# Optimization experiments

Measured on AMD Instinct MI355X. Metric: run time of the kernel, lower is better.

## Reference

```python
import jax, jax.numpy as jnp
import numpy as np

N = 131072          # total nodes per batched graph side
E = 524288          # total edges per batched graph side (avg degree 4)
B = 4096            # number of graph pairs
NPG = 32            # nodes per graph
NEG_SLOPE = 0.2
LN_EPS = 1e-5


def setup_inputs() -> dict:
    key = jax.random.key(0)
    ks = jax.random.split(key, 40)
    rn = lambda k, s, sc=0.05: jax.random.normal(k, s, dtype=jnp.float32) * sc
    inp = {}
    inp["feat1"] = jax.random.normal(ks[0], (N, 6), dtype=jnp.float32)
    inp["feat2"] = jax.random.normal(ks[1], (N, 6), dtype=jnp.float32)
    inp["llm_emb"] = jax.random.normal(ks[2], (B, 1024), dtype=jnp.float32)
    inp["src1"] = jax.random.randint(ks[3], (E,), 0, N, dtype=jnp.int32)
    inp["dst1"] = jax.random.randint(ks[4], (E,), 0, N, dtype=jnp.int32)
    inp["src2"] = jax.random.randint(ks[5], (E,), 0, N, dtype=jnp.int32)
    inp["dst2"] = jax.random.randint(ks[6], (E,), 0, N, dtype=jnp.int32)
    inp["gid"] = (jnp.arange(N, dtype=jnp.int32) // NPG).astype(jnp.int32)
    # shared GAT weights (layer: W[in,H*Dh], attn_l[H,Dh], attn_r[H,Dh], bias[H*Dh])
    inp["W1"] = rn(ks[7], (6, 128));   inp["al1"] = rn(ks[8], (4, 32));  inp["ar1"] = rn(ks[9], (4, 32));  inp["b1"] = rn(ks[10], (128,))
    inp["W2"] = rn(ks[11], (128, 128)); inp["al2"] = rn(ks[12], (4, 32)); inp["ar2"] = rn(ks[13], (4, 32)); inp["b2"] = rn(ks[14], (128,))
    inp["W3"] = rn(ks[15], (128, 256)); inp["al3"] = rn(ks[16], (4, 64)); inp["ar3"] = rn(ks[17], (4, 64)); inp["b3"] = rn(ks[18], (256,))
    # fusion
    inp["Wpg"] = rn(ks[19], (512, 512)); inp["bpg"] = rn(ks[20], (512,))
    inp["Wpl"] = rn(ks[21], (1024, 512)); inp["bpl"] = rn(ks[22], (512,))
    inp["Wv"] = rn(ks[23], (512, 512));  inp["bv"] = rn(ks[24], (512,))
    inp["Wo"] = rn(ks[25], (512, 512));  inp["bo"] = rn(ks[26], (512,))
    inp["gamma"] = jnp.ones((512,), jnp.float32); inp["beta"] = jnp.zeros((512,), jnp.float32)
    # classifier
    inp["Wc1"] = rn(ks[27], (512, 256)); inp["bc1"] = rn(ks[28], (256,))
    inp["Wc2"] = rn(ks[29], (256, 1));   inp["bc2"] = rn(ks[30], (1,))
    return inp


def _gat(x, src, dst, W, al, ar, b):
    # DGL GATConv: e_ij = LeakyReLU(a_l.h_src + a_r.h_dst), softmax over edges per dst
    H, Dh = al.shape
    h = (x @ W).reshape(-1, H, Dh)                 # [N,H,Dh]
    el = jnp.sum(h * al, axis=-1)                  # [N,H]
    er = jnp.sum(h * ar, axis=-1)                  # [N,H]
    e = jax.nn.leaky_relu(el[src] + er[dst], NEG_SLOPE)   # [E,H]
    m = jax.ops.segment_max(e, dst, num_segments=N)
    a = jnp.exp(e - m[dst])
    s = jax.ops.segment_sum(a, dst, num_segments=N)
    alpha = a / jnp.where(s[dst] == 0, 1.0, s[dst])       # [E,H]
    out = jax.ops.segment_sum(alpha[:, :, None] * h[src], dst, num_segments=N)
    return out.reshape(-1, H * Dh) + b


def _gnn(x, src, dst, gid, W1, al1, ar1, b1, W2, al2, ar2, b2, W3, al3, ar3, b3):
    h = jax.nn.relu(_gat(x, src, dst, W1, al1, ar1, b1))
    h = jax.nn.relu(_gat(h, src, dst, W2, al2, ar2, b2))
    h = _gat(h, src, dst, W3, al3, ar3, b3)        # [N,256]
    sums = jax.ops.segment_sum(h, gid, num_segments=B)
    cnt = jax.ops.segment_sum(jnp.ones((h.shape[0], 1), h.dtype), gid, num_segments=B)
    return sums / cnt                               # [B,256] mean_nodes


def reference(feat1, feat2, llm_emb, src1, dst1, src2, dst2, gid,
              W1, al1, ar1, b1, W2, al2, ar2, b2, W3, al3, ar3, b3,
              Wpg, bpg, Wpl, bpl, Wv, bv, Wo, bo, gamma, beta,
              Wc1, bc1, Wc2, bc2):
    h1 = _gnn(feat1, src1, dst1, gid, W1, al1, ar1, b1, W2, al2, ar2, b2, W3, al3, ar3, b3)
    h2 = _gnn(feat2, src2, dst2, gid, W1, al1, ar1, b1, W2, al2, ar2, b2, W3, al3, ar3, b3)
    pair = jnp.concatenate([h1, h2], axis=1)        # [B,512]
    gp = pair @ Wpg + bpg                           # [B,512]
    lp = llm_emb @ Wpl + bpl                        # [B,512]
    # MHA with kv seq_len 1: softmax over a single key == 1 -> out = W_o(W_v gp)
    attn = (gp @ Wv + bv) @ Wo + bo
    x = attn + lp
    mu = jnp.mean(x, axis=-1, keepdims=True)
    var = jnp.mean((x - mu) ** 2, axis=-1, keepdims=True)
    fused = (x - mu) / jnp.sqrt(var + LN_EPS) * gamma + beta
    hcls = jax.nn.relu(fused @ Wc1 + bc1)
    return jax.nn.sigmoid(hcls @ Wc2 + bc2)         # [B,1]
```

## Files before the change

kernel.cpp:

```cpp
#include <hip/hip_runtime.h>
#include <hip/hip_fp8.h>

#define NN 131072
#define NE 524288
#define NB 4096
#define CAP 16
#define NEG_SLOPE 0.2f
#define LN_EPS 1e-5f
#define LOG2E 1.44269504088896f

#define NBKT 1024
#define NBLK1 256
#define CELL_CAP 24

typedef unsigned short bf16;
typedef __attribute__((ext_vector_type(8))) short short8;
typedef __attribute__((ext_vector_type(4))) float floatx4;
typedef __attribute__((ext_vector_type(2))) float floatx2;

#if __has_builtin(__builtin_amdgcn_exp2f)
#define EXP2(x) __builtin_amdgcn_exp2f(x)
#else
#define EXP2(x) exp2f(x)
#endif

__device__ __forceinline__ float bf2f(bf16 h) {
    return __uint_as_float((unsigned)h << 16);
}
__device__ __forceinline__ bf16 f2bf(float f) {
    unsigned u = __float_as_uint(f);
    unsigned r = (u + 0x7FFFu + ((u >> 16) & 1u)) >> 16;
    return (bf16)r;
}
__device__ __forceinline__ unsigned pkbf(float lo, float hi) {
    unsigned r;
    asm("v_cvt_pk_bf16_f32 %0, %1, %2" : "=v"(r) : "v"(lo), "v"(hi));
    return r;
}
__device__ __forceinline__ unsigned char ftofp8(float f) {
    return (unsigned char)(__builtin_amdgcn_cvt_pk_fp8_f32(f, f, 0, false) & 0xFF);
}
__device__ __forceinline__ float leaky(float x) {
    return fmaxf(x, 0.f) + NEG_SLOPE * fminf(x, 0.f);
}

__global__ __launch_bounds__(256) void part_edges_kernel(
        const int* __restrict__ s0, const int* __restrict__ d0,
        const int* __restrict__ s1, const int* __restrict__ d1,
        unsigned* __restrict__ cells, int* __restrict__ counts) {
    __shared__ int lcnt[NBKT];
    int blk = blockIdx.x, t = threadIdx.x;
    for (int i = t; i < NBKT; i += 256) lcnt[i] = 0;
    __syncthreads();
    int side = blk >= (NBLK1 / 2);
    const int4* dp = (const int4*)(side ? d1 : d0);
    const int4* sp = (const int4*)(side ? s1 : s0);
    int base4 = (blk - side * (NBLK1 / 2)) * 1024;
    int gbase = side * NN;
#pragma unroll
    for (int it = 0; it < 4; it++) {
        int e4 = base4 + it * 256 + t;
        int4 dd = dp[e4];
        int4 ss = sp[e4];
        int d[4] = {gbase + dd.x, gbase + dd.y, gbase + dd.z, gbase + dd.w};
        int s[4] = {gbase + ss.x, gbase + ss.y, gbase + ss.z, gbase + ss.w};
#pragma unroll
        for (int k = 0; k < 4; k++) {
            int b = d[k] >> 8;
            int r = atomicAdd(&lcnt[b], 1);
            if (r < CELL_CAP)
                cells[((size_t)b * NBLK1 + blk) * CELL_CAP + r] =
                    ((unsigned)s[k] << 8) | (unsigned)(d[k] & 255);
        }
    }
    __syncthreads();
    for (int i = t; i < NBKT; i += 256) {
        int c = lcnt[i];
        counts[i * NBLK1 + blk] = (c > CELL_CAP) ? CELL_CAP : c;
    }
}

__global__ __launch_bounds__(256) void build_slots_kernel(
        const unsigned* __restrict__ cells, const int* __restrict__ counts,
        int* __restrict__ deg, int* __restrict__ slots) {
    __shared__ int ldeg[256];
    __shared__ int lslot[256 * CAP];
    int b = blockIdx.x, t = threadIdx.x;
    ldeg[t] = 0;
    for (int i = t; i < 256 * CAP; i += 256) lslot[i] = 0;
    __syncthreads();
    int cnt = counts[b * NBLK1 + t];
    const unsigned* cp = cells + ((size_t)b * NBLK1 + t) * CELL_CAP;
    for (int i = 0; i < cnt; i++) {
        unsigned v = cp[i];
        int d = v & 255;
        int s = (int)(v >> 8);
        int p = atomicAdd(&ldeg[d], 1);
        if (p < CAP) lslot[d * CAP + p] = s;
    }
    __syncthreads();
    int node0 = b * 256;
    deg[node0 + t] = ldeg[t];
    for (int i = t; i < 256 * CAP; i += 256)
        slots[(size_t)node0 * CAP + i] = lslot[i];
}

#define PREP_TOTAL (16384 + 32768 + 524288 + 131072 + 2048 + 2048 + 48 + 4096)

__global__ void prep_all_kernel(const float* __restrict__ W2, const float* __restrict__ W3,
                                const float* __restrict__ Wpl, const float* __restrict__ Wc1,
                                const float* __restrict__ W1,
                                const float* __restrict__ al1, const float* __restrict__ ar1,
                                const float* __restrict__ al2, const float* __restrict__ ar2,
                                const float* __restrict__ al3, const float* __restrict__ ar3,
                                const float* __restrict__ b1v,
                                bf16* __restrict__ W2t, bf16* __restrict__ W3t,
                                bf16* __restrict__ Wplt, bf16* __restrict__ Wc1t,
                                bf16* __restrict__ Ff2, bf16* __restrict__ Ff3,
                                float* __restrict__ F1, bf16* __restrict__ W1f) {
    int i = blockIdx.x * blockDim.x + threadIdx.x;
    if (i < 16384) {
        int c = i >> 7, k = i & 127;
        W2t[i] = f2bf(W2[k * 128 + c]);
        return;
    }
    i -= 16384;
    if (i < 32768) {
        int c = i >> 7, k = i & 127;
        W3t[i] = f2bf(W3[k * 256 + c]);
        return;
    }
    i -= 32768;
    if (i < 524288) {
        int c = i >> 10, k = i & 1023;
        Wplt[i] = f2bf(Wpl[k * 512 + c]);
        return;
    }
    i -= 524288;
    if (i < 131072) {
        int c = i >> 9, k = i & 511;
        Wc1t[i] = f2bf(Wc1[k * 256 + c]);
        return;
    }
    i -= 131072;
    if (i < 2048) {
        int c = i >> 7, k = i & 127;
        float s = 0.f;
        if (c < 8) {
            const float* a = (c < 4) ? al2 : ar2;
            int hh = c & 3;
            for (int d = 0; d < 32; d++) s += W2[k * 128 + hh * 32 + d] * a[hh * 32 + d];
        }
        Ff2[i] = f2bf(s);
        return;
    }
    i -= 2048;
    if (i < 2048) {
        int c = i >> 7, k = i & 127;
        float s = 0.f;
        if (c < 8) {
            const float* a = (c < 4) ? al3 : ar3;
            int hh = c & 3;
            for (int d = 0; d < 64; d++) s += W3[k * 256 + hh * 64 + d] * a[hh * 64 + d];
        }
        Ff3[i] = f2bf(s);
        return;
    }
    i -= 2048;
    if (i < 48) {
        int k = i >> 3, c = i & 7;
        const float* a = (c < 4) ? al1 : ar1;
        int hh = c & 3;
        float s = 0.f;
        for (int d = 0; d < 32; d++) s += W1[k * 128 + hh * 32 + d] * a[hh * 32 + d];
        F1[k * 8 + c] = s * LOG2E;
        return;
    }
    i -= 48;
    if (i < 4096) {
        int c = i >> 5, k = i & 31;
        int h = c >> 5, d = k & 7;
        float v = 0.f;
        if ((k >> 3) == h) {
            if (d < 6) v = W1[d * 128 + c];
            else if (d == 6) v = b1v[c];
        }
        W1f[i] = f2bf(v);
    }
}

__global__ void f2bf_kernel(const float* __restrict__ x, bf16* __restrict__ y) {
    int i = blockIdx.x * blockDim.x + threadIdx.x;
    float4 v = ((const float4*)x)[i];
    ushort4 u;
    u.x = f2bf(v.x); u.y = f2bf(v.y); u.z = f2bf(v.z); u.w = f2bf(v.w);
    ((ushort4*)y)[i] = u;
}

__global__ void wt_kernel(const float* __restrict__ W, bf16* __restrict__ Wt, int K, int C) {
    int i = blockIdx.x * blockDim.x + threadIdx.x;
    if (i >= K * C) return;
    int c = i / K, k = i - c * K;
    Wt[i] = f2bf(W[(size_t)k * C + c]);
}


__global__ void featelr_kernel(const float* __restrict__ f0, const float* __restrict__ f1,
                               const float* __restrict__ F1, float* __restrict__ fpk,
                               float* __restrict__ el, float* __restrict__ er) {
    int n = blockIdx.x * blockDim.x + threadIdx.x;
    const float* x = (n < NN) ? (f0 + (size_t)n * 6) : (f1 + (size_t)(n - NN) * 6);
    float xv[6];
#pragma unroll
    for (int k = 0; k < 6; k++) xv[k] = x[k];
    float4* o = (float4*)(fpk + (size_t)n * 8);
    o[0] = make_float4(xv[0], xv[1], xv[2], xv[3]);
    o[1] = make_float4(xv[4], xv[5], 0.f, 0.f);
    float4 elv, erv;
    float* ep = (float*)&elv;
    float* rp = (float*)&erv;
#pragma unroll
    for (int c = 0; c < 4; c++) {
        float sl = 0.f, sr = 0.f;
#pragma unroll
        for (int k = 0; k < 6; k++) {
            sl += xv[k] * F1[k * 8 + c];
            sr += xv[k] * F1[k * 8 + c + 4];
        }
        ep[c] = sl;
        rp[c] = sr;
    }
    *(float4*)(el + (size_t)n * 4) = elv;
    *(float4*)(er + (size_t)n * 4) = erv;
}

__global__ __launch_bounds__(256) void agg1mfma_kernel(
        const float* __restrict__ fpk, const float* __restrict__ el,
        const float* __restrict__ er, const int* __restrict__ deg,
        const int* __restrict__ slots, const bf16* __restrict__ W1fg,
        bf16* __restrict__ xb) {
    __shared__ bf16 sW[128 * 40];
    __shared__ bf16 sagg[256 * 40];
    int t = threadIdx.x;
    if (t < 128) {
        const uint4* src = (const uint4*)(W1fg + t * 32);
        uint4* dstp = (uint4*)(sW + t * 40);
        dstp[0] = src[0]; dstp[1] = src[1]; dstp[2] = src[2]; dstp[3] = src[3];
    }

    int node = blockIdx.x * 256 + t;
    int dg = deg[node];
    dg = (dg > CAP) ? CAP : dg;
    float4 er4 = *(const float4*)(er + (size_t)node * 4);
    const int* sp = slots + (size_t)node * CAP;
    float a0[4], a1[4], a2[4], a3[4], a4[4], a5[4], ss[4];
#pragma unroll
    for (int h = 0; h < 4; h++) {
        a0[h] = a1[h] = a2[h] = a3[h] = a4[h] = a5[h] = ss[h] = 0.f;
    }
    for (int p = 0; p < dg; p += 4) {
        int4 s4 = *(const int4*)(sp + p);
        int sarr[4] = {s4.x, s4.y, s4.z, s4.w};
#pragma unroll
        for (int k = 0; k < 4; k++) {
            bool vld = (p + k) < dg;
            int g = vld ? sarr[k] : s4.x;
            float4 e4 = *(const float4*)(el + (size_t)g * 4);
            float4 xa = *(const float4*)(fpk + (size_t)g * 8);
            float4 xc = *(const float4*)(fpk + (size_t)g * 8 + 4);
            float eh[4] = {e4.x, e4.y, e4.z, e4.w};
            float rh[4] = {er4.x, er4.y, er4.z, er4.w};
#pragma unroll
            for (int h = 0; h < 4; h++) {
                float z = eh[h] + rh[h];
                float w = EXP2(fmaxf(z, 0.f) + NEG_SLOPE * fminf(z, 0.f));
                w = vld ? w : 0.f;
                ss[h] += w;
                a0[h] += w * xa.x; a1[h] += w * xa.y; a2[h] += w * xa.z;
                a3[h] += w * xa.w; a4[h] += w * xc.x; a5[h] += w * xc.y;
            }
        }
    }
#pragma unroll
    for (int h = 0; h < 4; h++) {
        float rs = (dg > 0) ? 1.f / ss[h] : 0.f;
        uint4 o;
        o.x = pkbf(a0[h] * rs, a1[h] * rs);
        o.y = pkbf(a2[h] * rs, a3[h] * rs);
        o.z = pkbf(a4[h] * rs, a5[h] * rs);
        o.w = 0x00003F80u;
        *(uint4*)(sagg + t * 40 + h * 8) = o;
    }
    __syncthreads();

    int wave = t >> 6, lane = t & 63;
    int mlane = lane & 15, quad = lane >> 4;
    short8 af[8];
#pragma unroll
    for (int j = 0; j < 8; j++)
        af[j] = *(const short8*)(sW + (j * 16 + mlane) * 40 + quad * 8);
    floatx4 z4 = (floatx4){0.f, 0.f, 0.f, 0.f};
#pragma unroll
    for (int nt = 0; nt < 4; nt++) {
        int lrow = wave * 64 + nt * 16 + mlane;
        short8 bfr = *(const short8*)(sagg + lrow * 40 + quad * 8);
        floatx4 c[8];
#pragma unroll
        for (int j = 0; j < 8; j++)
            c[j] = __builtin_amdgcn_mfma_f32_16x16x32_bf16(af[j], bfr, z4, 0, 0, 0);
        bf16* op = xb + (size_t)(blockIdx.x * 256 + lrow) * 128 + quad * 4;
#pragma unroll
        for (int j = 0; j < 8; j++) {
            uint2 o;
            o.x = pkbf(fmaxf(c[j][0], 0.f), fmaxf(c[j][1], 0.f));
            o.y = pkbf(fmaxf(c[j][2], 0.f), fmaxf(c[j][3], 0.f));
            *(uint2*)(op + j * 16) = o;
        }
    }
}


__device__ __forceinline__ void softmax_phaseA(const float* __restrict__ el,
                                               const float* __restrict__ er,
                                               const int* __restrict__ slots,
                                               int wid, int dg, int lane,
                                               float* alpha_out, int* src_out) {
    int e = lane & 15, h = lane >> 4;
    int sA = slots[(size_t)wid * CAP + e];
    int sAc = (e < dg) ? sA : 0;
    float erh = er[wid * 4 + h];
    float elv = el[sAc * 4 + h];
    float w = (e < dg) ? __expf(leaky(elv + erh)) : 0.f;
    float ssum = w;
    ssum += __shfl_xor(ssum, 1, 64);
    ssum += __shfl_xor(ssum, 2, 64);
    ssum += __shfl_xor(ssum, 4, 64);
    ssum += __shfl_xor(ssum, 8, 64);
    *alpha_out = (dg > 0) ? w * (1.f / ssum) : 0.f;
    *src_out = sAc;
}

__global__ void agg2_kernel(const unsigned char* __restrict__ h8, const float* __restrict__ el,
                            const float* __restrict__ er, const int* __restrict__ deg,
                            const int* __restrict__ slots, const float* __restrict__ bias,
                            bf16* __restrict__ out) {
    int t = blockIdx.x * blockDim.x + threadIdx.x;
    int wid = t >> 5;
    int gl = threadIdx.x & 31;
    int dg = deg[wid];
    dg = (dg > CAP) ? CAP : dg;
    int head = gl >> 3;
    int fbase = gl * 4;
    float erh = er[wid * 4 + head];
    const int* sp = slots + (size_t)wid * CAP;
    float a0 = 0.f, a1 = 0.f, a2 = 0.f, a3 = 0.f, ssum = 0.f;

    for (int p = 0; p < dg; p += 4) {
        int4 s4 = *(const int4*)(sp + p);
        int s[4]; bool v[4];
        s[0] = s4.x; v[0] = true;
        v[1] = p + 1 < dg; s[1] = v[1] ? s4.y : s4.x;
        v[2] = p + 2 < dg; s[2] = v[2] ? s4.z : s4.x;
        v[3] = p + 3 < dg; s[3] = v[3] ? s4.w : s4.x;
        float elv[4]; unsigned u1[4];
#pragma unroll
        for (int k = 0; k < 4; k++) {
            elv[k] = el[s[k] * 4 + head];
            u1[k] = *(const unsigned*)(h8 + (size_t)s[k] * 128 + fbase);
        }
#pragma unroll
        for (int k = 0; k < 4; k++) {
            float w = v[k] ? __expf(leaky(elv[k] + erh)) : 0.f;
            ssum += w;
            floatx2 lo = __builtin_amdgcn_cvt_pk_f32_fp8((int)u1[k], false);
            floatx2 hi = __builtin_amdgcn_cvt_pk_f32_fp8((int)u1[k], true);
            a0 += w * lo[0]; a1 += w * lo[1];
            a2 += w * hi[0]; a3 += w * hi[1];
        }
    }
    float rs = (dg > 0) ? 1.f / ssum : 0.f;
    float4 bbv = *(const float4*)(bias + fbase);
    float v0 = fmaxf(a0 * rs + bbv.x, 0.f), v1 = fmaxf(a1 * rs + bbv.y, 0.f);
    float v2 = fmaxf(a2 * rs + bbv.z, 0.f), v3 = fmaxf(a3 * rs + bbv.w, 0.f);
    uint2 uo;
    uo.x = (unsigned)f2bf(v0) | ((unsigned)f2bf(v1) << 16);
    uo.y = (unsigned)f2bf(v2) | ((unsigned)f2bf(v3) << 16);
    *(uint2*)(out + (size_t)wid * 128 + fbase) = uo;
}

__global__ void agg3pool_kernel(const unsigned char* __restrict__ h8,
                                const float* __restrict__ el, const float* __restrict__ er,
                                const int* __restrict__ deg, const int* __restrict__ slots,
                                const float* __restrict__ bias, bf16* __restrict__ pair) {
    __shared__ float red[4 * 256];
    int side = blockIdx.x >> 12;
    int b = blockIdx.x & 4095;
    int nodebase = side * NN + b * 32;
    int grp = threadIdx.x >> 6, lane = threadIdx.x & 63;
    int fbase = lane * 4;
    int grpbase = lane & 48;
    float p0 = 0.f, p1 = 0.f, p2 = 0.f, p3 = 0.f;

    for (int nn = 0; nn < 8; nn++) {
        int wid = nodebase + grp * 8 + nn;
        int dg = deg[wid];
        dg = (dg > CAP) ? CAP : dg;
        float alpha; int sAc;
        softmax_phaseA(el, er, slots, wid, dg, lane, &alpha, &sAc);
        for (int p = 0; p < dg; p += 4) {
            int sc[4]; float av[4];
#pragma unroll
            for (int k = 0; k < 4; k++) {
                int srcl = grpbase + p + k;
                sc[k] = __shfl(sAc, srcl, 64);
                av[k] = __shfl(alpha, srcl, 64);
            }
            unsigned u[4];
#pragma unroll
            for (int k = 0; k < 4; k++)
                u[k] = *(const unsigned*)(h8 + (size_t)sc[k] * 256 + fbase);
#pragma unroll
            for (int k = 0; k < 4; k++) {
                floatx2 lo = __builtin_amdgcn_cvt_pk_f32_fp8((int)u[k], false);
                floatx2 hi = __builtin_amdgcn_cvt_pk_f32_fp8((int)u[k], true);
                p0 += av[k] * lo[0]; p1 += av[k] * lo[1];
                p2 += av[k] * hi[0]; p3 += av[k] * hi[1];
            }
        }
    }
    red[grp * 256 + fbase + 0] = p0;
    red[grp * 256 + fbase + 1] = p1;
    red[grp * 256 + fbase + 2] = p2;
    red[grp * 256 + fbase + 3] = p3;
    __syncthreads();
    if (grp == 0) {
        float4 bbv = *(const float4*)(bias + fbase);
        float s0 = 0.f, s1 = 0.f, s2 = 0.f, s3 = 0.f;
#pragma unroll
        for (int g = 0; g < 4; g++) {
            s0 += red[g * 256 + fbase + 0];
            s1 += red[g * 256 + fbase + 1];
            s2 += red[g * 256 + fbase + 2];
            s3 += red[g * 256 + fbase + 3];
        }
        const float inv = 1.0f / 32.0f;
        float v0 = s0 * inv + bbv.x, v1 = s1 * inv + bbv.y;
        float v2 = s2 * inv + bbv.z, v3 = s3 * inv + bbv.w;
        uint2 uo;
        uo.x = (unsigned)f2bf(v0) | ((unsigned)f2bf(v1) << 16);
        uo.y = (unsigned)f2bf(v2) | ((unsigned)f2bf(v3) << 16);
        *(uint2*)(pair + (size_t)b * 512 + side * 256 + fbase) = uo;
    }
}

template <bool FOLD, bool OUT8>
__global__ __launch_bounds__(256) void mgemm_kernel(const bf16* __restrict__ A,
                                                    const bf16* __restrict__ Wt,
                                                    const float* __restrict__ bias,
                                                    void* __restrict__ out,
                                                    int K, int C, int relu,
                                                    const bf16* __restrict__ Ff,
                                                    float* __restrict__ el,
                                                    float* __restrict__ er) {
    __shared__ short As[128 * 48];
    __shared__ short Bs[128 * 48];
    int t = threadIdx.x;
    int wave = t >> 6, lane = t & 63;
    int wm = (wave >> 1) * 64, wn = (wave & 1) * 64;
    int bm = blockIdx.x * 128, bn = blockIdx.y * 128;
    int m_lane = lane & 15, quad = lane >> 4;
    bool dofold = FOLD && (blockIdx.y == 0) && (wn == 0);

    floatx4 acc[4][4];
#pragma unroll
    for (int i = 0; i < 4; i++)
#pragma unroll
        for (int j = 0; j < 4; j++) acc[i][j] = (floatx4){0.f, 0.f, 0.f, 0.f};
    floatx4 facc[4];
    if (FOLD) {
#pragma unroll
        for (int i = 0; i < 4; i++) facc[i] = (floatx4){0.f, 0.f, 0.f, 0.f};
    }

    int lrow = t >> 2, lq = t & 3;
    for (int k0 = 0; k0 < K; k0 += 32) {
        __syncthreads();
#pragma unroll
        for (int pass = 0; pass < 2; pass++) {
            int row = lrow + pass * 64;
            *(short8*)&As[row * 48 + lq * 8] =
                *(const short8*)(A + (size_t)(bm + row) * K + k0 + lq * 8);
            *(short8*)&Bs[row * 48 + lq * 8] =
                *(const short8*)(Wt + (size_t)(bn + row) * K + k0 + lq * 8);
        }
        __syncthreads();
        short8 af[4], bf[4];
#pragma unroll
        for (int i = 0; i < 4; i++)
            af[i] = *(const short8*)&As[(wm + i * 16 + m_lane) * 48 + quad * 8];
#pragma unroll
        for (int j = 0; j < 4; j++)
            bf[j] = *(const short8*)&Bs[(wn + j * 16 + m_lane) * 48 + quad * 8];
        if (dofold) {
            short8 fbv = *(const short8*)(Ff + m_lane * K + k0 + quad * 8);
#pragma unroll
            for (int i = 0; i < 4; i++)
                facc[i] = __builtin_amdgcn_mfma_f32_16x16x32_bf16(af[i], fbv, facc[i], 0, 0, 0);
        }
#pragma unroll
        for (int i = 0; i < 4; i++)
#pragma unroll
            for (int j = 0; j < 4; j++)
                acc[i][j] = __builtin_amdgcn_mfma_f32_16x16x32_bf16(af[i], bf[j], acc[i][j], 0, 0, 0);
    }

#pragma unroll
    for (int i = 0; i < 4; i++) {
#pragma unroll
        for (int j = 0; j < 4; j++) {
            int gc = bn + wn + j * 16 + m_lane;
            float bbv = bias ? bias[gc] : 0.f;
#pragma unroll
            for (int r = 0; r < 4; r++) {
                int gr = bm + wm + i * 16 + quad * 4 + r;
                float v = acc[i][j][r] + bbv;
                if (relu) v = fmaxf(v, 0.f);
                if (OUT8) ((unsigned char*)out)[(size_t)gr * C + gc] = ftofp8(v);
                else      ((bf16*)out)[(size_t)gr * C + gc] = f2bf(v);
            }
        }
    }
    if (dofold && m_lane < 8) {
        float* dst = (m_lane < 4) ? el : er;
        int hh = m_lane & 3;
#pragma unroll
        for (int i = 0; i < 4; i++)
#pragma unroll
            for (int r = 0; r < 4; r++) {
                int gr = bm + wm + i * 16 + quad * 4 + r;
                dst[gr * 4 + hh] = facc[i][r];
            }
    }
}

__global__ __launch_bounds__(256) void fgemm512_kernel(const float* __restrict__ A,
                                                       const float* __restrict__ B,
                                                       float* __restrict__ C) {
    const int BK = 16;
    __shared__ float As[BK][68];
    __shared__ float Bs[BK][68];
    int t = threadIdx.x;
    int bm = blockIdx.x * 64, bn = blockIdx.y * 64;
    int tm0 = (t & 15) * 4, tn0 = (t >> 4) * 4;
    float acc[4][4] = {};
    int la_m = t >> 2, la_k = (t & 3) * 4;
    int lb_k = t >> 4, lb_c = (t & 15) * 4;

    for (int k0 = 0; k0 < 512; k0 += BK) {
        float4 a4 = *(const float4*)(A + (size_t)(bm + la_m) * 512 + k0 + la_k);
        float4 b4 = *(const float4*)(B + (size_t)(k0 + lb_k) * 512 + bn + lb_c);
        As[la_k + 0][la_m] = a4.x; As[la_k + 1][la_m] = a4.y;
        As[la_k + 2][la_m] = a4.z; As[la_k + 3][la_m] = a4.w;
        *(float4*)&Bs[lb_k][lb_c] = b4;
        __syncthreads();
#pragma unroll
        for (int k = 0; k < BK; k++) {
            float4 av = *(const float4*)&As[k][tm0];
            float4 bv = *(const float4*)&Bs[k][tn0];
            acc[0][0] += av.x * bv.x; acc[0][1] += av.x * bv.y; acc[0][2] += av.x * bv.z; acc[0][3] += av.x * bv.w;
            acc[1][0] += av.y * bv.x; acc[1][1] += av.y * bv.y; acc[1][2] += av.y * bv.z; acc[1][3] += av.y * bv.w;
            acc[2][0] += av.z * bv.x; acc[2][1] += av.z * bv.y; acc[2][2] += av.z * bv.z; acc[2][3] += av.z * bv.w;
            acc[3][0] += av.w * bv.x; acc[3][1] += av.w * bv.y; acc[3][2] += av.w * bv.z; acc[3][3] += av.w * bv.w;
        }
        __syncthreads();
    }
#pragma unroll
    for (int i = 0; i < 4; i++) {
        float4 o = make_float4(acc[i][0], acc[i][1], acc[i][2], acc[i][3]);
        *(float4*)(C + (size_t)(bm + tm0 + i) * 512 + bn + tn0) = o;
    }
}

__global__ void biasstep_kernel(const float* __restrict__ vin, const float* __restrict__ M,
                                const float* __restrict__ badd, float* __restrict__ vout) {
    int c = blockIdx.x * blockDim.x + threadIdx.x;
    float s = 0.f;
    for (int k = 0; k < 512; k++) s += vin[k] * M[(size_t)k * 512 + c];
    vout[c] = s + badd[c];
}


__global__ void ln_kernel(const bf16* __restrict__ attn, const bf16* __restrict__ lp,
                          const float* __restrict__ gamma, const float* __restrict__ beta,
                          bf16* __restrict__ out) {
    __shared__ float red[256];
    int b = blockIdx.x, t = threadIdx.x;
    size_t base = (size_t)b * 512;
    float x0 = bf2f(attn[base + t]) + bf2f(lp[base + t]);
    float x1 = bf2f(attn[base + 256 + t]) + bf2f(lp[base + 256 + t]);
    red[t] = x0 + x1; __syncthreads();
    for (int off = 128; off > 0; off >>= 1) { if (t < off) red[t] += red[t + off]; __syncthreads(); }
    float mu = red[0] * (1.0f / 512.0f);
    __syncthreads();
    float d0 = x0 - mu, d1 = x1 - mu;
    red[t] = d0 * d0 + d1 * d1; __syncthreads();
    for (int off = 128; off > 0; off >>= 1) { if (t < off) red[t] += red[t + off]; __syncthreads(); }
    float rstd = rsqrtf(red[0] * (1.0f / 512.0f) + LN_EPS);
    out[base + t]       = f2bf(d0 * rstd * gamma[t] + beta[t]);
    out[base + 256 + t] = f2bf(d1 * rstd * gamma[256 + t] + beta[256 + t]);
}

__global__ void cls2_kernel(const bf16* __restrict__ hc, const float* __restrict__ Wc2,
                            const float* __restrict__ bc2, float* __restrict__ out) {
    int wid = (blockIdx.x * blockDim.x + threadIdx.x) >> 6;
    int lane = threadIdx.x & 63;
    if (wid >= NB) return;
    float s = 0.f;
#pragma unroll
    for (int j = 0; j < 4; j++) {
        int k = lane + 64 * j;
        s += bf2f(hc[(size_t)wid * 256 + k]) * Wc2[k];
    }
    for (int off = 32; off > 0; off >>= 1) s += __shfl_down(s, off);
    if (lane == 0) {
        float v = s + bc2[0];
        out[wid] = 1.0f / (1.0f + __expf(-v));
    }
}


static inline size_t alup(size_t x) { return (x + 255) & ~(size_t)255; }

extern "C" void kernel_launch(void* const* d_in, const int* in_sizes, int n_in,
                              void* d_out, int out_size, void* d_ws, size_t ws_size,
                              hipStream_t stream) {
    const float* feat0 = (const float*)d_in[0];
    const float* feat1 = (const float*)d_in[1];
    const float* llm = (const float*)d_in[2];
    const int* srcs[2] = {(const int*)d_in[3], (const int*)d_in[5]};
    const int* dsts[2] = {(const int*)d_in[4], (const int*)d_in[6]};
    const float* W1 = (const float*)d_in[8];
    const float* al[3] = {(const float*)d_in[9],  (const float*)d_in[13], (const float*)d_in[17]};
    const float* ar[3] = {(const float*)d_in[10], (const float*)d_in[14], (const float*)d_in[18]};
    const float* bb[3] = {(const float*)d_in[11], (const float*)d_in[15], (const float*)d_in[19]};
    const float* W2 = (const float*)d_in[12];
    const float* W3 = (const float*)d_in[16];
    const float* Wpg = (const float*)d_in[20]; const float* bpg = (const float*)d_in[21];
    const float* Wpl = (const float*)d_in[22]; const float* bpl = (const float*)d_in[23];
    const float* Wv  = (const float*)d_in[24]; const float* bv  = (const float*)d_in[25];
    const float* Wo  = (const float*)d_in[26]; const float* bo  = (const float*)d_in[27];
    const float* gamma = (const float*)d_in[28]; const float* beta = (const float*)d_in[29];
    const float* Wc1 = (const float*)d_in[30]; const float* bc1 = (const float*)d_in[31];
    const float* Wc2 = (const float*)d_in[32]; const float* bc2 = (const float*)d_in[33];
    float* outp = (float*)d_out;

    const size_t N2 = (size_t)2 * NN;

    char* p = (char*)d_ws;
    auto take = [&](size_t bytes) { char* r = p; p += alup(bytes); return r; };
    bf16*  xb     = (bf16*)take(N2 * 128 * 2);
    char*  regB   = (char*)take(N2 * 256);
    float* el     = (float*)take(N2 * 4 * 4);
    float* er     = (float*)take(N2 * 4 * 4);
    int*   deg    = (int*)take(N2 * 4);
    int*   slots  = (int*)take(N2 * CAP * 4);
    bf16*  pair   = (bf16*)take((size_t)NB * 512 * 2);
    bf16*  llm_bf = (bf16*)take((size_t)NB * 1024 * 2);
    bf16*  W2t  = (bf16*)take(128 * 128 * 2);
    bf16*  W3t  = (bf16*)take(128 * 256 * 2);
    bf16*  Wplt = (bf16*)take(1024 * 512 * 2);
    bf16*  Wc1t = (bf16*)take(512 * 256 * 2);
    bf16*  Wcot = (bf16*)take(512 * 512 * 2);
    float* F1   = (float*)take(6 * 8 * 4);
    bf16*  Ff2  = (bf16*)take(16 * 128 * 2);
    bf16*  Ff3  = (bf16*)take(16 * 128 * 2);
    bf16*  W1fg = (bf16*)take(128 * 32 * 2);
    float* c1   = (float*)take(512 * 512 * 4);
    float* c2   = (float*)take(512 * 512 * 4);
    float* bias1 = (float*)take(512 * 4);
    float* bco   = (float*)take(512 * 4);
    unsigned* cells = (unsigned*)regB;
    int* counts = (int*)(regB + (size_t)NBKT * NBLK1 * CELL_CAP * 4);
    float* fpk          = (float*)regB;
    unsigned char* hb2  = (unsigned char*)regB;
    unsigned char* hb3  = (unsigned char*)regB;
    bf16* fbb   = (bf16*)regB;
    bf16* lp    = fbb + (size_t)0 * NB * 512;
    bf16* attn  = fbb + (size_t)1 * NB * 512;
    bf16* fused = fbb + (size_t)2 * NB * 512;
    bf16* hc    = fbb + (size_t)3 * NB * 512;
    (void)ws_size; (void)n_in; (void)in_sizes; (void)out_size;

    auto mgemm = [&](const bf16* A, const bf16* Wt, const float* bias, bf16* o,
                     int M, int K, int C, int relu) {
        dim3 g(M / 128, C / 128);
        mgemm_kernel<false, false><<<g, 256, 0, stream>>>(A, Wt, bias, o, K, C, relu,
                                                          nullptr, nullptr, nullptr);
    };

    part_edges_kernel<<<NBLK1, 256, 0, stream>>>(srcs[0], dsts[0], srcs[1], dsts[1],
                                                 cells, counts);
    build_slots_kernel<<<NBKT, 256, 0, stream>>>(cells, counts, deg, slots);

    prep_all_kernel<<<(PREP_TOTAL + 255) / 256, 256, 0, stream>>>(
        W2, W3, Wpl, Wc1, W1, al[0], ar[0], al[1], ar[1], al[2], ar[2], bb[0],
        W2t, W3t, Wplt, Wc1t, Ff2, Ff3, F1, W1fg);
    f2bf_kernel<<<NB * 1024 / 4 / 256, 256, 0, stream>>>(llm, llm_bf);
    {
        dim3 g8(8, 8);
        fgemm512_kernel<<<g8, 256, 0, stream>>>(Wpg, Wv, c1);
        fgemm512_kernel<<<g8, 256, 0, stream>>>(c1, Wo, c2);
        wt_kernel<<<(512 * 512 + 255) / 256, 256, 0, stream>>>(c2, Wcot, 512, 512);
        biasstep_kernel<<<2, 256, 0, stream>>>(bpg, Wv, bv, bias1);
        biasstep_kernel<<<2, 256, 0, stream>>>(bias1, Wo, bo, bco);
    }

    featelr_kernel<<<2 * NN / 256, 256, 0, stream>>>(feat0, feat1, F1, fpk, el, er);
    agg1mfma_kernel<<<2 * NN / 256, 256, 0, stream>>>(fpk, el, er, deg, slots, W1fg, xb);
    {
        dim3 g(2 * NN / 128, 1);
        mgemm_kernel<true, true><<<g, 256, 0, stream>>>(xb, W2t, nullptr, hb2, 128, 128, 0,
                                                        Ff2, el, er);
    }
    agg2_kernel<<<2 * NN * 32 / 256, 256, 0, stream>>>(hb2, el, er, deg, slots, bb[1], xb);
    {
        dim3 g(2 * NN / 128, 2);
        mgemm_kernel<true, true><<<g, 256, 0, stream>>>(xb, W3t, nullptr, hb3, 128, 256, 0,
                                                        Ff3, el, er);
    }
    agg3pool_kernel<<<2 * NB, 256, 0, stream>>>(hb3, el, er, deg, slots, bb[2], pair);

    mgemm(llm_bf, Wplt, bpl, lp, NB, 1024, 512, 0);
    mgemm(pair, Wcot, bco, attn, NB, 512, 512, 0);
    ln_kernel<<<NB, 256, 0, stream>>>(attn, lp, gamma, beta, fused);
    mgemm(fused, Wc1t, bc1, hc, NB, 512, 256, 1);
    cls2_kernel<<<NB / 4, 256, 0, stream>>>(hc, Wc2, bc2, outp);
}
```

Baseline: 580.1 us.

## Reorder layer-3 GAT: aggregate before projection, pool then apply block-diagonal W3

Layer 3 now aggregates the 128-dim layer-2 output per head (stored as fp8) and mean-pools per graph first. Only then does it apply W3, as a small block-diagonal GEMM over pooled per-head features that writes straight into the pair layout. This removes the large per-node 128x256 GEMM and halves the gather width in the layer-3 aggregation. Attention logits come from a new small MFMA kernel using the folded attention vectors. The cost is extra fp8 quantization of layer-2 output and per-head accumulators (4x channels) in the pooling kernel.

Measured after the change: 570.9 us. Within noise of the previous version (-1.6%).

```diff
diff --git a/kernel.cpp b/kernel.cpp
--- a/kernel.cpp
+++ b/kernel.cpp
@@ -105,7 +105,7 @@
         slots[(size_t)node0 * CAP + i] = lslot[i];
 }
 
-#define PREP_TOTAL (16384 + 32768 + 524288 + 131072 + 2048 + 2048 + 48 + 4096)
+#define PREP_TOTAL (16384 + 524288 + 131072 + 2048 + 2048 + 48 + 4096 + 131072)
 
 __global__ void prep_all_kernel(const float* __restrict__ W2, const float* __restrict__ W3,
                                 const float* __restrict__ Wpl, const float* __restrict__ Wc1,
@@ -114,10 +114,11 @@
                                 const float* __restrict__ al2, const float* __restrict__ ar2,
                                 const float* __restrict__ al3, const float* __restrict__ ar3,
                                 const float* __restrict__ b1v,
-                                bf16* __restrict__ W2t, bf16* __restrict__ W3t,
-                                bf16* __restrict__ Wplt, bf16* __restrict__ Wc1t,
+                                bf16* __restrict__ W2t, bf16* __restrict__ Wplt,
+                                bf16* __restrict__ Wc1t,
                                 bf16* __restrict__ Ff2, bf16* __restrict__ Ff3,
-                                float* __restrict__ F1, bf16* __restrict__ W1f) {
+                                float* __restrict__ F1, bf16* __restrict__ W1f,
+                                bf16* __restrict__ W3bdt) {
     int i = blockIdx.x * blockDim.x + threadIdx.x;
     if (i < 16384) {
         int c = i >> 7, k = i & 127;
@@ -125,12 +126,6 @@
         return;
     }
     i -= 16384;
-    if (i < 32768) {
-        int c = i >> 7, k = i & 127;
-        W3t[i] = f2bf(W3[k * 256 + c]);
-        return;
-    }
-    i -= 32768;
     if (i < 524288) {
         int c = i >> 10, k = i & 1023;
         Wplt[i] = f2bf(Wpl[k * 512 + c]);
@@ -186,6 +181,14 @@
             else if (d == 6) v = b1v[c];
         }
         W1f[i] = f2bf(v);
+        return;
+    }
+    i -= 4096;
+    if (i < 131072) {
+        int c = i >> 9, r = i & 511;
+        int hr = r >> 7, k = r & 127;
+        float v = (hr == (c >> 6)) ? W3[k * 256 + c] : 0.f;
+        W3bdt[i] = f2bf(v);
     }
 }
 
@@ -343,7 +346,7 @@
 __global__ void agg2_kernel(const unsigned char* __restrict__ h8, const float* __restrict__ el,
                             const float* __restrict__ er, const int* __restrict__ deg,
                             const int* __restrict__ slots, const float* __restrict__ bias,
-                            bf16* __restrict__ out) {
+                            unsigned char* __restrict__ out) {
     int t = blockIdx.x * blockDim.x + threadIdx.x;
     int wid = t >> 5;
     int gl = threadIdx.x & 31;
@@ -382,24 +385,63 @@
     float4 bbv = *(const float4*)(bias + fbase);
     float v0 = fmaxf(a0 * rs + bbv.x, 0.f), v1 = fmaxf(a1 * rs + bbv.y, 0.f);
     float v2 = fmaxf(a2 * rs + bbv.z, 0.f), v3 = fmaxf(a3 * rs + bbv.w, 0.f);
-    uint2 uo;
-    uo.x = (unsigned)f2bf(v0) | ((unsigned)f2bf(v1) << 16);
-    uo.y = (unsigned)f2bf(v2) | ((unsigned)f2bf(v3) << 16);
-    *(uint2*)(out + (size_t)wid * 128 + fbase) = uo;
-}
-
-__global__ void agg3pool_kernel(const unsigned char* __restrict__ h8,
+    unsigned w8 = (unsigned)__builtin_amdgcn_cvt_pk_fp8_f32(v0, v1, 0, false);
+    w8 = (unsigned)__builtin_amdgcn_cvt_pk_fp8_f32(v2, v3, (int)w8, true);
+    *(unsigned*)(out + (size_t)wid * 128 + fbase) = w8;
+}
+
+__global__ __launch_bounds__(256) void elr3_kernel(const unsigned char* __restrict__ x8,
+                                                   const bf16* __restrict__ Ff3,
+                                                   float* __restrict__ el,
+                                                   float* __restrict__ er) {
+    int wave = threadIdx.x >> 6, lane = threadIdx.x & 63;
+    int mlane = lane & 15, quad = lane >> 4;
+    int node0 = blockIdx.x * 64 + wave * 16;
+    floatx4 acc = (floatx4){0.f, 0.f, 0.f, 0.f};
+#pragma unroll
+    for (int kb = 0; kb < 4; kb++) {
+        short8 bfr = *(const short8*)(Ff3 + mlane * 128 + kb * 32 + quad * 8);
+        uint2 u8 = *(const uint2*)(x8 + (size_t)(node0 + mlane) * 128 + kb * 32 + quad * 8);
+        floatx2 f01 = __builtin_amdgcn_cvt_pk_f32_fp8((int)u8.x, false);
+        floatx2 f23 = __builtin_amdgcn_cvt_pk_f32_fp8((int)u8.x, true);
+        floatx2 f45 = __builtin_amdgcn_cvt_pk_f32_fp8((int)u8.y, false);
+        floatx2 f67 = __builtin_amdgcn_cvt_pk_f32_fp8((int)u8.y, true);
+        short8 af;
+        unsigned* ap = (unsigned*)&af;
+        ap[0] = pkbf(f01[0], f01[1]); ap[1] = pkbf(f23[0], f23[1]);
+        ap[2] = pkbf(f45[0], f45[1]); ap[3] = pkbf(f67[0], f67[1]);
+        acc = __builtin_amdgcn_mfma_f32_16x16x32_bf16(af, bfr, acc, 0, 0, 0);
+    }
+    if (mlane < 8) {
+        float* dst = (mlane < 4) ? el : er;
+        int h = mlane & 3;
+#pragma unroll
+        for (int r = 0; r < 4; r++) {
+            int node = node0 + quad * 4 + r;
+            dst[node * 4 + h] = acc[r];
+        }
+    }
+}
+
+__global__ void agg3pool_kernel(const unsigned char* __restrict__ x8,
                                 const float* __restrict__ el, const float* __restrict__ er,
                                 const int* __restrict__ deg, const int* __restrict__ slots,
-                                const float* __restrict__ bias, bf16* __restrict__ pair) {
-    __shared__ float red[4 * 256];
+                                bf16* __restrict__ poolagg) {
+    __shared__ float red[4][4][128];
+    __shared__ float salpha[4][16][4];
+    __shared__ int   ssrc[4][16];
     int side = blockIdx.x >> 12;
     int b = blockIdx.x & 4095;
     int nodebase = side * NN + b * 32;
     int grp = threadIdx.x >> 6, lane = threadIdx.x & 63;
-    int fbase = lane * 4;
-    int grpbase = lane & 48;
-    float p0 = 0.f, p1 = 0.f, p2 = 0.f, p3 = 0.f;
+    int e = lane & 15, h = lane >> 4;
+    int esl = lane >> 5;
+    int ch4 = (lane & 31) * 4;
+    float acc[4][4];
+#pragma unroll
+    for (int hh = 0; hh < 4; hh++)
+#pragma unroll
+        for (int c = 0; c < 4; c++) acc[hh][c] = 0.f;
 
     for (int nn = 0; nn < 8; nn++) {
         int wid = nodebase + grp * 8 + nn;
@@ -407,53 +449,58 @@
         dg = (dg > CAP) ? CAP : dg;
         float alpha; int sAc;
         softmax_phaseA(el, er, slots, wid, dg, lane, &alpha, &sAc);
+        salpha[grp][e][h] = alpha;
+        if (h == 0) ssrc[grp][e] = sAc;
         for (int p = 0; p < dg; p += 4) {
-            int sc[4]; float av[4];
-#pragma unroll
-            for (int k = 0; k < 4; k++) {
-                int srcl = grpbase + p + k;
-                sc[k] = __shfl(sAc, srcl, 64);
-                av[k] = __shfl(alpha, srcl, 64);
-            }
-            unsigned u[4];
-#pragma unroll
-            for (int k = 0; k < 4; k++)
-                u[k] = *(const unsigned*)(h8 + (size_t)sc[k] * 256 + fbase);
-#pragma unroll
-            for (int k = 0; k < 4; k++) {
-                floatx2 lo = __builtin_amdgcn_cvt_pk_f32_fp8((int)u[k], false);
-                floatx2 hi = __builtin_amdgcn_cvt_pk_f32_fp8((int)u[k], true);
-                p0 += av[k] * lo[0]; p1 += av[k] * lo[1];
-                p2 += av[k] * hi[0]; p3 += av[k] * hi[1];
-            }
-        }
-    }
-    red[grp * 256 + fbase + 0] = p0;
-    red[grp * 256 + fbase + 1] = p1;
-    red[grp * 256 + fbase + 2] = p2;
-    red[grp * 256 + fbase + 3] = p3;
+            int ee0 = p + esl, ee1 = p + 2 + esl;
+            int s0 = ssrc[grp][ee0];
+            int s1 = ssrc[grp][ee1];
+            float4 av0 = *(const float4*)&salpha[grp][ee0][0];
+            float4 av1 = *(const float4*)&salpha[grp][ee1][0];
+            unsigned u0 = *(const unsigned*)(x8 + (size_t)s0 * 128 + ch4);
+            unsigned u1 = *(const unsigned*)(x8 + (size_t)s1 * 128 + ch4);
+            floatx2 lo0 = __builtin_amdgcn_cvt_pk_f32_fp8((int)u0, false);
+            floatx2 hi0 = __builtin_amdgcn_cvt_pk_f32_fp8((int)u0, true);
+            floatx2 lo1 = __builtin_amdgcn_cvt_pk_f32_fp8((int)u1, false);
+            floatx2 hi1 = __builtin_amdgcn_cvt_pk_f32_fp8((int)u1, true);
+            float xv0[4] = {lo0[0], lo0[1], hi0[0], hi0[1]};
+            float xv1[4] = {lo1[0], lo1[1], hi1[0], hi1[1]};
+            float aa0[4] = {av0.x, av0.y, av0.z, av0.w};
+            float aa1[4] = {av1.x, av1.y, av1.z, av1.w};
+#pragma unroll
+            for (int hh = 0; hh < 4; hh++)
+#pragma unroll
+                for (int c = 0; c < 4; c++)
+                    acc[hh][c] += aa0[hh] * xv0[c] + aa1[hh] * xv1[c];
+        }
+    }
+#pragma unroll
+    for (int hh = 0; hh < 4; hh++)
+#pragma unroll
+        for (int c = 0; c < 4; c++)
+            acc[hh][c] += __shfl_xor(acc[hh][c], 32, 64);
+    if (lane < 32) {
+#pragma unroll
+        for (int hh = 0; hh < 4; hh++)
+            *(float4*)&red[grp][hh][ch4] =
+                make_float4(acc[hh][0], acc[hh][1], acc[hh][2], acc[hh][3]);
+    }
     __syncthreads();
-    if (grp == 0) {
-        float4 bbv = *(const float4*)(bias + fbase);
-        float s0 = 0.f, s1 = 0.f, s2 = 0.f, s3 = 0.f;
-#pragma unroll
-        for (int g = 0; g < 4; g++) {
-            s0 += red[g * 256 + fbase + 0];
-            s1 += red[g * 256 + fbase + 1];
-            s2 += red[g * 256 + fbase + 2];
-            s3 += red[g * 256 + fbase + 3];
-        }
-        const float inv = 1.0f / 32.0f;
-        float v0 = s0 * inv + bbv.x, v1 = s1 * inv + bbv.y;
-        float v2 = s2 * inv + bbv.z, v3 = s3 * inv + bbv.w;
-        uint2 uo;
-        uo.x = (unsigned)f2bf(v0) | ((unsigned)f2bf(v1) << 16);
-        uo.y = (unsigned)f2bf(v2) | ((unsigned)f2bf(v3) << 16);
-        *(uint2*)(pair + (size_t)b * 512 + side * 256 + fbase) = uo;
-    }
-}
-
-template <bool FOLD, bool OUT8>
+    int t = threadIdx.x;
+    int hlo = t >> 7, c = t & 127;
+    float s0 = 0.f, s1 = 0.f;
+#pragma unroll
+    for (int g = 0; g < 4; g++) {
+        s0 += red[g][hlo][c];
+        s1 += red[g][2 + hlo][c];
+    }
+    const float inv = 1.0f / 32.0f;
+    size_t gbase = (size_t)(b * 2 + side) * 512;
+    poolagg[gbase + t] = f2bf(s0 * inv);
+    poolagg[gbase + t + 256] = f2bf(s1 * inv);
+}
+
+template <bool FOLD, bool OUT8, bool PAIR>
 __global__ __launch_bounds__(256) void mgemm_kernel(const bf16* __restrict__ A,
                                                     const bf16* __restrict__ Wt,
                                                     const float* __restrict__ bias,
@@ -525,8 +572,9 @@
                 int gr = bm + wm + i * 16 + quad * 4 + r;
                 float v = acc[i][j][r] + bbv;
                 if (relu) v = fmaxf(v, 0.f);
-                if (OUT8) ((unsigned char*)out)[(size_t)gr * C + gc] = ftofp8(v);
-                else      ((bf16*)out)[(size_t)gr * C + gc] = f2bf(v);
+                if (OUT8)      ((unsigned char*)out)[(size_t)gr * C + gc] = ftofp8(v);
+                else if (PAIR) ((bf16*)out)[(size_t)(gr >> 1) * 512 + (gr & 1) * 256 + gc] = f2bf(v);
+                else           ((bf16*)out)[(size_t)gr * C + gc] = f2bf(v);
             }
         }
     }
@@ -667,10 +715,10 @@
     bf16*  pair   = (bf16*)take((size_t)NB * 512 * 2);
     bf16*  llm_bf = (bf16*)take((size_t)NB * 1024 * 2);
     bf16*  W2t  = (bf16*)take(128 * 128 * 2);
-    bf16*  W3t  = (bf16*)take(128 * 256 * 2);
     bf16*  Wplt = (bf16*)take(1024 * 512 * 2);
     bf16*  Wc1t = (bf16*)take(512 * 256 * 2);
     bf16*  Wcot = (bf16*)take(512 * 512 * 2);
+    bf16*  W3bdt = (bf16*)take(256 * 512 * 2);
     float* F1   = (float*)take(6 * 8 * 4);
     bf16*  Ff2  = (bf16*)take(16 * 128 * 2);
     bf16*  Ff3  = (bf16*)take(16 * 128 * 2);
@@ -679,11 +727,12 @@
     float* c2   = (float*)take(512 * 512 * 4);
     float* bias1 = (float*)take(512 * 4);
     float* bco   = (float*)take(512 * 4);
+    unsigned char* x8 = (unsigned char*)xb;
     unsigned* cells = (unsigned*)regB;
     int* counts = (int*)(regB + (size_t)NBKT * NBLK1 * CELL_CAP * 4);
     float* fpk          = (float*)regB;
     unsigned char* hb2  = (unsigned char*)regB;
-    unsigned char* hb3  = (unsigned char*)regB;
+    bf16* poolagg = (bf16*)(regB + 32 * 1024 * 1024);
     bf16* fbb   = (bf16*)regB;
     bf16* lp    = fbb + (size_t)0 * NB * 512;
     bf16* attn  = fbb + (size_t)1 * NB * 512;
@@ -694,8 +743,8 @@
     auto mgemm = [&](const bf16* A, const bf16* Wt, const float* bias, bf16* o,
                      int M, int K, int C, int relu) {
         dim3 g(M / 128, C / 128);
-        mgemm_kernel<false, false><<<g, 256, 0, stream>>>(A, Wt, bias, o, K, C, relu,
-                                                          nullptr, nullptr, nullptr);
+        mgemm_kernel<false, false, false><<<g, 256, 0, stream>>>(A, Wt, bias, o, K, C, relu,
+                                                                 nullptr, nullptr, nullptr);
     };
 
     part_edges_kernel<<<NBLK1, 256, 0, stream>>>(srcs[0], dsts[0], srcs[1], dsts[1],
@@ -704,7 +753,7 @@
 
     prep_all_kernel<<<(PREP_TOTAL + 255) / 256, 256, 0, stream>>>(
         W2, W3, Wpl, Wc1, W1, al[0], ar[0], al[1], ar[1], al[2], ar[2], bb[0],
-        W2t, W3t, Wplt, Wc1t, Ff2, Ff3, F1, W1fg);
+        W2t, Wplt, Wc1t, Ff2, Ff3, F1, W1fg, W3bdt);
     f2bf_kernel<<<NB * 1024 / 4 / 256, 256, 0, stream>>>(llm, llm_bf);
     {
         dim3 g8(8, 8);
@@ -719,16 +768,18 @@
     agg1mfma_kernel<<<2 * NN / 256, 256, 0, stream>>>(fpk, el, er, deg, slots, W1fg, xb);
     {
         dim3 g(2 * NN / 128, 1);
-        mgemm_kernel<true, true><<<g, 256, 0, stream>>>(xb, W2t, nullptr, hb2, 128, 128, 0,
-                                                        Ff2, el, er);
-    }
-    agg2_kernel<<<2 * NN * 32 / 256, 256, 0, stream>>>(hb2, el, er, deg, slots, bb[1], xb);
+        mgemm_kernel<true, true, false><<<g, 256, 0, stream>>>(xb, W2t, nullptr, hb2,
+                                                               128, 128, 0, Ff2, el, er);
+    }
+    agg2_kernel<<<2 * NN * 32 / 256, 256, 0, stream>>>(hb2, el, er, deg, slots, bb[1], x8);
+    elr3_kernel<<<2 * NN / 64, 256, 0, stream>>>(x8, Ff3, el, er);
+    agg3pool_kernel<<<2 * NB, 256, 0, stream>>>(x8, el, er, deg, slots, poolagg);
     {
-        dim3 g(2 * NN / 128, 2);
-        mgemm_kernel<true, true><<<g, 256, 0, stream>>>(xb, W3t, nullptr, hb3, 128, 256, 0,
-                                                        Ff3, el, er);
-    }
-    agg3pool_kernel<<<2 * NB, 256, 0, stream>>>(hb3, el, er, deg, slots, bb[2], pair);
+        dim3 g(8192 / 128, 256 / 128);
+        mgemm_kernel<false, false, true><<<g, 256, 0, stream>>>(poolagg, W3bdt, bb[2], pair,
+                                                                512, 256, 0,
+                                                                nullptr, nullptr, nullptr);
+    }
 
     mgemm(llm_bf, Wplt, bpl, lp, NB, 1024, 512, 0);
     mgemm(pair, Wcot, bco, attn, NB, 512, 512, 0);
```
